# Optimization experiments

Measured on AMD Instinct MI355X. Metric: run time of the kernel, lower is better.

The kernel has to match this reference:

```python
import jax, jax.numpy as jnp
import numpy as np
from jax import lax

DN = ('NHWC', 'HWIO', 'NHWC')


def _conv(x, w, b=None, stride=1):
    y = lax.conv_general_dilated(x, w, (stride, stride), 'SAME', dimension_numbers=DN)
    return y + b if b is not None else y


def _conv_t(x, w, b, stride=2):
    y = lax.conv_transpose(x, w, (stride, stride), 'SAME', dimension_numbers=DN)
    return y + b


def _res_stack(x, blocks):
    # ResidualBlock: x + Conv1x1(relu(Conv3x3(relu(x)))); final relu after stack
    for w1, w2 in blocks:
        t = jax.nn.relu(x)
        t = _conv(t, w1)          # 3x3, no bias
        t = jax.nn.relu(t)
        t = _conv(t, w2)          # 1x1, no bias
        x = x + t
    return jax.nn.relu(x)


def setup_inputs() -> dict:
    key = jax.random.key(0)
    ks = jax.random.split(key, 32)
    s = 0.05
    n = lambda i, shape: jax.random.normal(ks[i], shape, dtype=jnp.float32) * s
    H, RH, D, K = 128, 32, 128, 512
    return {
        'x': jax.random.normal(ks[0], (16, 256, 256, 3), dtype=jnp.float32),
        'emb': jax.random.normal(ks[1], (K, D), dtype=jnp.float32),  # stddev 1.0 init
        'enc_w1': n(2, (4, 4, 3, H // 2)),  'enc_b1': jnp.zeros((H // 2,), jnp.float32),
        'enc_w2': n(3, (4, 4, H // 2, H)),  'enc_b2': jnp.zeros((H,), jnp.float32),
        'enc_w3': n(4, (3, 3, H, H)),       'enc_b3': jnp.zeros((H,), jnp.float32),
        'erb1_w1': n(5, (3, 3, H, RH)), 'erb1_w2': n(6, (1, 1, RH, H)),
        'erb2_w1': n(7, (3, 3, H, RH)), 'erb2_w2': n(8, (1, 1, RH, H)),
        'dec_w': n(9, (3, 3, D, H)),        'dec_b': jnp.zeros((H,), jnp.float32),
        'drb1_w1': n(10, (3, 3, H, RH)), 'drb1_w2': n(11, (1, 1, RH, H)),
        'drb2_w1': n(12, (3, 3, H, RH)), 'drb2_w2': n(13, (1, 1, RH, H)),
        'dt1_w': n(14, (4, 4, H, H // 2)),  'dt1_b': jnp.zeros((H // 2,), jnp.float32),
        'dt2_w': n(15, (4, 4, H // 2, 3)),  'dt2_b': jnp.zeros((3,), jnp.float32),
    }


def _forward(x, emb, enc_w1, enc_b1, enc_w2, enc_b2, enc_w3, enc_b3,
             erb1_w1, erb1_w2, erb2_w1, erb2_w2,
             dec_w, dec_b, drb1_w1, drb1_w2, drb2_w1, drb2_w2,
             dt1_w, dt1_b, dt2_w, dt2_b):
    f = jax.nn.relu(_conv(x, enc_w1, enc_b1, 2))
    f = jax.nn.relu(_conv(f, enc_w2, enc_b2, 2))
    f = _conv(f, enc_w3, enc_b3, 1)
    f = _res_stack(f, [(erb1_w1, erb1_w2), (erb2_w1, erb2_w2)])
    # VQ: full [N, K] squared-distance matrix, argmin, codebook gather
    D = emb.shape[1]
    flat = f.reshape(-1, D)                                   # [N, D]
    dist = ((flat ** 2).sum(axis=1, keepdims=True)
            + (emb ** 2).sum(axis=1)[None, :]
            - 2.0 * flat @ emb.T)                              # [N, K]
    idx = jnp.argmin(dist, axis=1)                             # [N]
    q = emb[idx].reshape(f.shape)                              # quantized
    y = _conv(q, dec_w, dec_b, 1)
    y = _res_stack(y, [(drb1_w1, drb1_w2), (drb2_w1, drb2_w2)])
    y = jax.nn.relu(_conv_t(y, dt1_w, dt1_b))
    y = _conv_t(y, dt2_w, dt2_b)
    return (y, f, q)


def reference(x, emb, enc_w1, enc_b1, enc_w2, enc_b2, enc_w3, enc_b3,
              erb1_w1, erb1_w2, erb2_w1, erb2_w2,
              dec_w, dec_b, drb1_w1, drb1_w2, drb2_w1, drb2_w2,
              dt1_w, dt1_b, dt2_w, dt2_b):
    return _forward(x, emb, enc_w1, enc_b1, enc_w2, enc_b2, enc_w3, enc_b3,
                    erb1_w1, erb1_w2, erb2_w1, erb2_w2,
                    dec_w, dec_b, drb1_w1, drb1_w2, drb2_w1, drb2_w2,
                    dt1_w, dt1_b, dt2_w, dt2_b)
```

## Files before the change

kernel.cpp:

```cpp
#include <hip/hip_runtime.h>
#include <hip/hip_bf16.h>
#include <hip/hip_fp16.h>

using bf16 = __hip_bfloat16;
using frag_ab = __attribute__((ext_vector_type(8))) short;
using f16x8  = __attribute__((ext_vector_type(8))) _Float16;
using frag_cd = __attribute__((ext_vector_type(4))) float;

enum { F_INRELU = 1, F_OUTRELU = 2, F_RES = 4 };

struct TapSet { int dy[16]; int dx[16]; int wi[16]; };

__device__ __forceinline__ unsigned int relu_pk(unsigned int v) {
    unsigned int m = ((v & 0x80008000u) >> 15) * 0xFFFFu;
    return v & ~m;
}
__device__ __forceinline__ unsigned int mask_by(unsigned int v, unsigned int h) {
    unsigned int m = ((h & 0x80008000u) >> 15) * 0xFFFFu;
    return v & ~m;
}

__global__ void pack_w_k(const float* __restrict__ w, bf16* __restrict__ dst,
                         int Ci, int Co, int BN, TapSet taps, int total)
{
    int idx = blockIdx.x * 256 + threadIdx.x;
    if (idx >= total) return;
    int j  = idx & 7;
    int r1 = idx >> 3;
    int nl = r1 % BN;
    int r2 = r1 / BN;
    int q  = r2 & 3;
    int cb = r2 >> 2;
    int nblocks = Co / BN;
    int c  = cb / nblocks;
    int nb = cb - c * nblocks;
    int cpt = Ci >> 5;
    int tap = c / cpt;
    int ci  = (c - tap * cpt) * 32 + q * 8 + j;
    int n   = nb * BN + nl;
    dst[idx] = __float2bfloat16(w[(size_t)(taps.wi[tap] * Ci + ci) * Co + n]);
}

__global__ void pack_w2_k(const float* __restrict__ w, __half* __restrict__ dst,
                          int Ci, int Co, int BN, TapSet taps, int total)
{
    int idx = blockIdx.x * 256 + threadIdx.x;
    if (idx >= total) return;
    int j  = idx & 7;
    int r1 = idx >> 3;
    int nl = r1 % BN;
    int r2 = r1 / BN;
    int q  = r2 & 3;
    int cb = r2 >> 2;
    int nblocks = Co / BN;
    int c  = cb / nblocks;
    int nb = cb - c * nblocks;
    int cpt = Ci >> 5;
    int tap = c / cpt;
    int ci  = (c - tap * cpt) * 32 + q * 8 + j;
    int n   = nb * BN + nl;
    float v = w[(size_t)(taps.wi[tap] * Ci + ci) * Co + n];
    __half h = __float2half(v);
    __half l = __float2half((v - __half2float(h)) * 2048.0f);
    size_t base = (size_t)cb * (BN * 64) + (q * BN + nl) * 8 + j;
    dst[base] = h;
    dst[base + BN * 32] = l;
}

__global__ void pack_wdt2_k(const float* __restrict__ w, __half* __restrict__ dst)
{
    int idx = blockIdx.x * 256 + threadIdx.x;
    if (idx >= 16384) return;
    int parity = idx >> 12;
    int r0 = idx & 4095;
    int j  = r0 & 7;
    int r1 = r0 >> 3;
    int nl = r1 & 15;
    int r2 = r1 >> 4;
    int q  = r2 & 3;
    int cb = r2 >> 2;
    int tap = cb >> 1;
    int cc  = cb & 1;
    int ci  = cc * 32 + q * 8 + j;
    int n   = nl;
    int py = parity >> 1, px = parity & 1;
    int ty = tap >> 1, tx = tap & 1;
    int wi = (py + 2 * ty) * 4 + (px + 2 * tx);
    float v = (n < 3) ? w[(size_t)(wi * 64 + ci) * 3 + n] : 0.f;
    __half h = __float2half(v);
    __half l = __float2half((v - __half2float(h)) * 2048.0f);
    size_t base = (size_t)parity * 8192 + cb * 1024 + (q * 16 + nl) * 8 + j;
    dst[base] = h;
    dst[base + 512] = l;
}

__global__ void pack_we1_k(const float* __restrict__ w, __half* __restrict__ dst)
{
    int idx = blockIdx.x * 256 + threadIdx.x;
    if (idx >= 4096) return;
    int j  = idx & 7;
    int r1 = idx >> 3;
    int nl = r1 & 63;
    int r2 = r1 >> 6;
    int q  = r2 & 3;
    int c  = r2 >> 2;
    int k  = c * 32 + q * 8 + j;
    int tap = k >> 2, ci = k & 3;
    float v = (ci < 3) ? w[(size_t)(tap * 3 + ci) * 64 + nl] : 0.f;
    __half h = __float2half(v);
    __half l = __float2half((v - __half2float(h)) * 2048.0f);
    size_t base = (size_t)c * 4096 + (q * 64 + nl) * 8 + j;
    dst[base] = h;
    dst[base + 2048] = l;
}

__global__ __launch_bounds__(256) void pad_x_k(
    const float* __restrict__ x, __half* __restrict__ xh, __half* __restrict__ xl)
{
    int pix = blockIdx.x * 256 + threadIdx.x;
    const float* ip = x + (size_t)pix * 3;
    float v0 = ip[0], v1 = ip[1], v2 = ip[2];
    unsigned short hb[4], lb[4];
    float vv[4] = {v0, v1, v2, 0.f};
#pragma unroll
    for (int i = 0; i < 4; ++i) {
        __half h = __float2half(vv[i]);
        hb[i] = __half_as_ushort(h);
        lb[i] = __half_as_ushort(__float2half((vv[i] - __half2float(h)) * 2048.0f));
    }
    uint2 hv = make_uint2((unsigned)hb[0] | ((unsigned)hb[1] << 16),
                          (unsigned)hb[2] | ((unsigned)hb[3] << 16));
    uint2 lv = make_uint2((unsigned)lb[0] | ((unsigned)lb[1] << 16),
                          (unsigned)lb[2] | ((unsigned)lb[3] << 16));
    *(uint2*)(xh + (size_t)pix * 4) = hv;
    *(uint2*)(xl + (size_t)pix * 4) = lv;
}

__global__ __launch_bounds__(256) void enc1_mfma_k(
    const __half* __restrict__ xh, const __half* __restrict__ xl,
    const __half* __restrict__ wp, const float* __restrict__ bias,
    __half* __restrict__ oh, __half* __restrict__ ol)
{
    __shared__ __align__(16) short Ash[64 * 32];
    __shared__ __align__(16) short Asl[64 * 32];
    __shared__ __align__(16) short Bsh[64 * 32];
    __shared__ __align__(16) short Bsl[64 * 32];

    const int tid = threadIdx.x;
    const int m0 = blockIdx.x * 64;

    const int am = tid >> 2;
    const int aq = tid & 3;
    const int gm  = m0 + am;
    const int nn_ = gm >> 14;
    const int rr_ = gm & 16383;
    const int iy0 = (rr_ >> 7) * 2 - 1;
    const int ix0 = (rr_ & 127) * 2 - 1;

    const int lane = tid & 63;
    const int wv4 = tid >> 6;
    const int wm = (wv4 & 1) * 32;
    const int wn = (wv4 >> 1) * 32;
    const int lm = lane & 15, lq = lane >> 4;

    frag_cd accA[2][2], accB[2][2];
#pragma unroll
    for (int i = 0; i < 2; ++i)
#pragma unroll
        for (int j = 0; j < 2; ++j)
#pragma unroll
            for (int r = 0; r < 4; ++r) { accA[i][j][r] = 0.f; accB[i][j][r] = 0.f; }

#pragma unroll
    for (int c = 0; c < 2; ++c) {
        const int tap = c * 8 + aq * 2;
        const int ky = tap >> 2, kx = tap & 3;
        const int iy = iy0 + ky;
        const int ix = ix0 + kx;
        uint2 h0 = make_uint2(0u, 0u), h1 = h0, l0 = h0, l1 = h0;
        if (iy >= 0 && iy < 256) {
            const size_t rowb = (size_t)(nn_ * 256 + iy) * 256;
            if (ix >= 0 && ix < 256) {
                h0 = *(const uint2*)(xh + (rowb + ix) * 4);
                l0 = *(const uint2*)(xl + (rowb + ix) * 4);
            }
            if (ix + 1 >= 0 && ix + 1 < 256) {
                h1 = *(const uint2*)(xh + (rowb + ix + 1) * 4);
                l1 = *(const uint2*)(xl + (rowb + ix + 1) * 4);
            }
        }
        __syncthreads();
        *(uint4*)&Ash[(aq * 64 + am) * 8] = make_uint4(h0.x, h0.y, h1.x, h1.y);
        *(uint4*)&Asl[(aq * 64 + am) * 8] = make_uint4(l0.x, l0.y, l1.x, l1.y);
        {
            const __half* wc = wp + (size_t)c * 4096;
            *(uint4*)&Bsh[tid * 8] = *(const uint4*)(wc + tid * 8);
            *(uint4*)&Bsl[tid * 8] = *(const uint4*)(wc + 2048 + tid * 8);
        }
        __syncthreads();

        f16x8 afh[2], afl[2], bfh[2], bfl[2];
#pragma unroll
        for (int i = 0; i < 2; ++i) {
            afh[i] = *(const f16x8*)&Ash[(lq * 64 + wm + i * 16 + lm) * 8];
            afl[i] = *(const f16x8*)&Asl[(lq * 64 + wm + i * 16 + lm) * 8];
        }
#pragma unroll
        for (int j = 0; j < 2; ++j) {
            bfh[j] = *(const f16x8*)&Bsh[(lq * 64 + wn + j * 16 + lm) * 8];
            bfl[j] = *(const f16x8*)&Bsl[(lq * 64 + wn + j * 16 + lm) * 8];
        }
#pragma unroll
        for (int i = 0; i < 2; ++i)
#pragma unroll
            for (int j = 0; j < 2; ++j) {
                accA[i][j] = __builtin_amdgcn_mfma_f32_16x16x32_f16(afh[i], bfh[j], accA[i][j], 0, 0, 0);
                accB[i][j] = __builtin_amdgcn_mfma_f32_16x16x32_f16(afh[i], bfl[j], accB[i][j], 0, 0, 0);
                accB[i][j] = __builtin_amdgcn_mfma_f32_16x16x32_f16(afl[i], bfh[j], accB[i][j], 0, 0, 0);
            }
    }

    const float s = 1.0f / 2048.0f;
#pragma unroll
    for (int j = 0; j < 2; ++j) {
        const int n_g = wn + j * 16 + lm;
        const float bv = bias[n_g];
#pragma unroll
        for (int i = 0; i < 2; ++i) {
#pragma unroll
            for (int r = 0; r < 4; ++r) {
                const int m_g = m0 + wm + i * 16 + lq * 4 + r;
                const size_t ob = (size_t)m_g * 64 + n_g;
                float v = accA[i][j][r] + accB[i][j][r] * s + bv;
                v = fmaxf(v, 0.f);
                __half h = __float2half(v);
                oh[ob] = h;
                ol[ob] = __float2half((v - __half2float(h)) * 2048.0f);
            }
        }
    }
}

template<int BN>
__global__ __launch_bounds__(256) void conv_mfma2_k(
    const __half* __restrict__ ah, const __half* __restrict__ al,
    const __half* __restrict__ wp, const float* __restrict__ bias,
    float* __restrict__ out, __half* __restrict__ oh, __half* __restrict__ ol,
    const __half* __restrict__ rh, const __half* __restrict__ rl,
    int IH, int IW, int Ci, int Co, int sy_in,
    TapSet taps, int ntaps, int flags)
{
    __shared__ __align__(16) short Ash[64 * 32];
    __shared__ __align__(16) short Asl[64 * 32];
    __shared__ __align__(16) short Bsh[BN * 32];
    __shared__ __align__(16) short Bsl[BN * 32];

    const int tid = threadIdx.x;
    const int m0 = blockIdx.x * 64;
    const int n0 = blockIdx.y * BN;

    const int am = tid >> 2;
    const int aq = tid & 3;
    const int gm  = m0 + am;
    const int nn_ = gm >> 12;
    const int rr_ = gm & 4095;
    const int oy_ = (rr_ >> 6) * sy_in;
    const int ox_ = (rr_ & 63) * sy_in;

    const int lane = tid & 63;
    const int wv4 = tid >> 6;
    constexpr int MT = (BN == 64) ? 2 : 1;
    constexpr int NT = 2;
    const int wm = (BN == 64) ? (wv4 & 1) * 32 : wv4 * 16;
    const int wn = (BN == 64) ? (wv4 >> 1) * 32 : 0;
    const int lm = lane & 15, lq = lane >> 4;
    constexpr int NLOAD = BN * 32 / 8;

    frag_cd accA[MT][NT], accB[MT][NT];
#pragma unroll
    for (int i = 0; i < MT; ++i)
#pragma unroll
        for (int j = 0; j < NT; ++j)
#pragma unroll
            for (int r = 0; r < 4; ++r) { accA[i][j][r] = 0.f; accB[i][j][r] = 0.f; }

    const int cpt = Ci >> 5;
    const int nch = ntaps * cpt;
    const bool inrelu = (flags & F_INRELU) != 0;

    int tap = 0, cc = 0, ci0 = 0;
    for (int c = 0; c < nch; ++c) {
        const int iy = oy_ + taps.dy[tap];
        const int ix = ox_ + taps.dx[tap];
        uint4 avh = make_uint4(0u, 0u, 0u, 0u);
        uint4 avl = make_uint4(0u, 0u, 0u, 0u);
        if (iy >= 0 && iy < IH && ix >= 0 && ix < IW) {
            const size_t off = (size_t)((nn_ * IH + iy) * IW + ix) * Ci + ci0 + aq * 8;
            avh = *(const uint4*)(ah + off);
            avl = *(const uint4*)(al + off);
        }
        if (inrelu) {
            avl.x = mask_by(avl.x, avh.x); avl.y = mask_by(avl.y, avh.y);
            avl.z = mask_by(avl.z, avh.z); avl.w = mask_by(avl.w, avh.w);
            avh.x = relu_pk(avh.x); avh.y = relu_pk(avh.y);
            avh.z = relu_pk(avh.z); avh.w = relu_pk(avh.w);
        }
        uint4 bvh, bvl;
        if (tid < NLOAD) {
            const __half* wc = wp + (size_t)(c * gridDim.y + blockIdx.y) * (BN * 64);
            bvh = *(const uint4*)(wc + tid * 8);
            bvl = *(const uint4*)(wc + BN * 32 + tid * 8);
        }

        __syncthreads();
        *(uint4*)&Ash[(aq * 64 + am) * 8] = avh;
        *(uint4*)&Asl[(aq * 64 + am) * 8] = avl;
        if (tid < NLOAD) {
            *(uint4*)&Bsh[tid * 8] = bvh;
            *(uint4*)&Bsl[tid * 8] = bvl;
        }
        __syncthreads();

        f16x8 afh[MT], afl[MT], bfh[NT], bfl[NT];
#pragma unroll
        for (int i = 0; i < MT; ++i) {
            afh[i] = *(const f16x8*)&Ash[(lq * 64 + wm + i * 16 + lm) * 8];
            afl[i] = *(const f16x8*)&Asl[(lq * 64 + wm + i * 16 + lm) * 8];
        }
#pragma unroll
        for (int j = 0; j < NT; ++j) {
            bfh[j] = *(const f16x8*)&Bsh[(lq * BN + wn + j * 16 + lm) * 8];
            bfl[j] = *(const f16x8*)&Bsl[(lq * BN + wn + j * 16 + lm) * 8];
        }
#pragma unroll
        for (int i = 0; i < MT; ++i)
#pragma unroll
            for (int j = 0; j < NT; ++j) {
                accA[i][j] = __builtin_amdgcn_mfma_f32_16x16x32_f16(afh[i], bfh[j], accA[i][j], 0, 0, 0);
                accB[i][j] = __builtin_amdgcn_mfma_f32_16x16x32_f16(afh[i], bfl[j], accB[i][j], 0, 0, 0);
                accB[i][j] = __builtin_amdgcn_mfma_f32_16x16x32_f16(afl[i], bfh[j], accB[i][j], 0, 0, 0);
            }

        ci0 += 32;
        if (++cc == cpt) { cc = 0; ci0 = 0; ++tap; }
    }

    const float s = 1.0f / 2048.0f;
#pragma unroll
    for (int j = 0; j < NT; ++j) {
        const int n_g = n0 + wn + j * 16 + lm;
        const float bv = bias ? bias[n_g] : 0.f;
#pragma unroll
        for (int i = 0; i < MT; ++i) {
#pragma unroll
            for (int r = 0; r < 4; ++r) {
                const int m_g = m0 + wm + i * 16 + lq * 4 + r;
                const size_t ob = (size_t)m_g * Co + n_g;
                float v = accA[i][j][r] + accB[i][j][r] * s + bv;
                if (flags & F_RES)
                    v += __half2float(rh[ob]) + __half2float(rl[ob]) * s;
                if (flags & F_OUTRELU) v = fmaxf(v, 0.f);
                if (out) out[ob] = v;
                if (oh) {
                    __half h = __float2half(v);
                    oh[ob] = h;
                    ol[ob] = __float2half((v - __half2float(h)) * 2048.0f);
                }
            }
        }
    }
}

template<int BN>
__global__ __launch_bounds__(256) void conv_mfma_k(
    const bf16* __restrict__ a, const bf16* __restrict__ wp,
    const float* __restrict__ bias,
    float* __restrict__ out, bf16* __restrict__ out_bf,
    const float* __restrict__ res,
    int Ci, int Co, int OHf, int OWf, int sy_out, int py, int px,
    TapSet taps, int ntaps, int flags)
{
    __shared__ __align__(16) short As[64 * 32];
    __shared__ __align__(16) short Bs[BN * 32];

    const int tid = threadIdx.x;
    const int m0 = blockIdx.x * 64;
    const int n0 = blockIdx.y * BN;

    const int am = tid >> 2;
    const int aq = tid & 3;
    const int gm  = m0 + am;
    const int nn_ = gm >> 12;
    const int rr_ = gm & 4095;
    const int oy_ = rr_ >> 6;
    const int ox_ = rr_ & 63;

    const int lane = tid & 63;
    const int wv4 = tid >> 6;
    constexpr int MT = (BN == 64) ? 2 : 1;
    constexpr int NT = 2;
    const int wm = (BN == 64) ? (wv4 & 1) * 32 : wv4 * 16;
    const int wn = (BN == 64) ? (wv4 >> 1) * 32 : 0;
    const int lm = lane & 15, lq = lane >> 4;
    constexpr int NLOAD = BN * 32 / 8;

    frag_cd acc[MT][NT];
#pragma unroll
    for (int i = 0; i < MT; ++i)
#pragma unroll
        for (int j = 0; j < NT; ++j)
#pragma unroll
            for (int r = 0; r < 4; ++r) acc[i][j][r] = 0.f;

    const int cpt = Ci >> 5;
    const int nch = ntaps * cpt;
    const bool inrelu = (flags & F_INRELU) != 0;

    int tap = 0, cc = 0, ci0 = 0;
    for (int c = 0; c < nch; ++c) {
        const int iy = oy_ + taps.dy[tap];
        const int ix = ox_ + taps.dx[tap];
        uint4 av = make_uint4(0u, 0u, 0u, 0u);
        if (iy >= 0 && iy < 64 && ix >= 0 && ix < 64)
            av = *(const uint4*)(a + (size_t)((nn_ * 64 + iy) * 64 + ix) * Ci + ci0 + aq * 8);
        if (inrelu) {
            av.x = relu_pk(av.x); av.y = relu_pk(av.y);
            av.z = relu_pk(av.z); av.w = relu_pk(av.w);
        }
        uint4 bv;
        if (tid < NLOAD)
            bv = *(const uint4*)(wp + ((size_t)c * gridDim.y + blockIdx.y) * (BN * 32) + tid * 8);

        __syncthreads();
        *(uint4*)&As[(aq * 64 + am) * 8] = av;
        if (tid < NLOAD) *(uint4*)&Bs[tid * 8] = bv;
        __syncthreads();

        frag_ab af[MT], bfr[NT];
#pragma unroll
        for (int i = 0; i < MT; ++i)
            af[i] = *(const frag_ab*)&As[(lq * 64 + wm + i * 16 + lm) * 8];
#pragma unroll
        for (int j = 0; j < NT; ++j)
            bfr[j] = *(const frag_ab*)&Bs[(lq * BN + wn + j * 16 + lm) * 8];
#pragma unroll
        for (int i = 0; i < MT; ++i)
#pragma unroll
            for (int j = 0; j < NT; ++j)
                acc[i][j] = __builtin_amdgcn_mfma_f32_16x16x32_bf16(af[i], bfr[j], acc[i][j], 0, 0, 0);

        ci0 += 32;
        if (++cc == cpt) { cc = 0; ci0 = 0; ++tap; }
    }

#pragma unroll
    for (int j = 0; j < NT; ++j) {
        const int n_g = n0 + wn + j * 16 + lm;
        const float bv = bias ? bias[n_g] : 0.f;
#pragma unroll
        for (int i = 0; i < MT; ++i) {
#pragma unroll
            for (int r = 0; r < 4; ++r) {
                const int m_g = m0 + wm + i * 16 + lq * 4 + r;
                const int nn2 = m_g >> 12;
                const int rr2 = m_g & 4095;
                const int oy = (rr2 >> 6) * sy_out + py;
                const int ox = (rr2 & 63) * sy_out + px;
                const size_t ob = ((size_t)(nn2 * OHf + oy) * OWf + ox) * Co + n_g;
                float v = acc[i][j][r] + bv;
                if (flags & F_RES)     v += res[ob];
                if (flags & F_OUTRELU) v = fmaxf(v, 0.f);
                if (out)    out[ob]    = v;
                if (out_bf) out_bf[ob] = __float2bfloat16(v);
            }
        }
    }
}

__global__ __launch_bounds__(256) void dt2_mfma_k(
    const float* __restrict__ in,
    const __half* __restrict__ wp,
    const float* __restrict__ bias,
    float* __restrict__ out)
{
    __shared__ __align__(16) short Ash[64 * 32];
    __shared__ __align__(16) short Asl[64 * 32];
    __shared__ __align__(16) short Bsh[16 * 32];
    __shared__ __align__(16) short Bsl[16 * 32];

    const int tid = threadIdx.x;
    const int par = blockIdx.x & 3;
    const int m0  = (blockIdx.x >> 2) * 64;
    const int py = par >> 1, px = par & 1;

    const int am = tid >> 2;
    const int aq = tid & 3;
    const int gm  = m0 + am;
    const int nn_ = gm >> 14;
    const int rr_ = gm & 16383;
    const int r_  = rr_ >> 7;
    const int c_  = rr_ & 127;

    const int lane = tid & 63;
    const int wv4 = tid >> 6;
    const int wm = wv4 * 16;
    const int lm = lane & 15, lq = lane >> 4;

    frag_cd accA, accB;
#pragma unroll
    for (int r = 0; r < 4; ++r) { accA[r] = 0.f; accB[r] = 0.f; }

    const __half* wpar = wp + (size_t)par * 8192;

    for (int c = 0; c < 8; ++c) {
        const int tap = c >> 1;
        const int iy = r_ + py + (tap >> 1) - 1;
        const int ix = c_ + px + (tap & 1) - 1;
        const int ci0 = (c & 1) * 32;
        uint4 hi = make_uint4(0u, 0u, 0u, 0u);
        uint4 lo = make_uint4(0u, 0u, 0u, 0u);
        if ((unsigned)iy < 128u && (unsigned)ix < 128u) {
            const float* ip = in + (size_t)((nn_ * 128 + iy) * 128 + ix) * 64 + ci0 + aq * 8;
            const float4 v0 = *(const float4*)ip;
            const float4 v1 = *(const float4*)(ip + 4);
            float vv[8] = {v0.x, v0.y, v0.z, v0.w, v1.x, v1.y, v1.z, v1.w};
            unsigned short hb[8], lb[8];
#pragma unroll
            for (int i = 0; i < 8; ++i) {
                __half h = __float2half(vv[i]);
                hb[i] = __half_as_ushort(h);
                lb[i] = __half_as_ushort(__float2half((vv[i] - __half2float(h)) * 2048.0f));
            }
            hi = make_uint4((unsigned)hb[0] | ((unsigned)hb[1] << 16),
                            (unsigned)hb[2] | ((unsigned)hb[3] << 16),
                            (unsigned)hb[4] | ((unsigned)hb[5] << 16),
                            (unsigned)hb[6] | ((unsigned)hb[7] << 16));
            lo = make_uint4((unsigned)lb[0] | ((unsigned)lb[1] << 16),
                            (unsigned)lb[2] | ((unsigned)lb[3] << 16),
                            (unsigned)lb[4] | ((unsigned)lb[5] << 16),
                            (unsigned)lb[6] | ((unsigned)lb[7] << 16));
        }
        uint4 bvh, bvl;
        if (tid < 64) {
            const __half* wc = wpar + c * 1024;
            bvh = *(const uint4*)(wc + tid * 8);
            bvl = *(const uint4*)(wc + 512 + tid * 8);
        }

        __syncthreads();
        *(uint4*)&Ash[(aq * 64 + am) * 8] = hi;
        *(uint4*)&Asl[(aq * 64 + am) * 8] = lo;
        if (tid < 64) {
            *(uint4*)&Bsh[tid * 8] = bvh;
            *(uint4*)&Bsl[tid * 8] = bvl;
        }
        __syncthreads();

        const f16x8 afh = *(const f16x8*)&Ash[(lq * 64 + wm + lm) * 8];
        const f16x8 afl = *(const f16x8*)&Asl[(lq * 64 + wm + lm) * 8];
        const f16x8 bfh = *(const f16x8*)&Bsh[(lq * 16 + lm) * 8];
        const f16x8 bfl = *(const f16x8*)&Bsl[(lq * 16 + lm) * 8];
        accA = __builtin_amdgcn_mfma_f32_16x16x32_f16(afh, bfh, accA, 0, 0, 0);
        accB = __builtin_amdgcn_mfma_f32_16x16x32_f16(afh, bfl, accB, 0, 0, 0);
        accB = __builtin_amdgcn_mfma_f32_16x16x32_f16(afl, bfh, accB, 0, 0, 0);
    }

    const float s = 1.0f / 2048.0f;
    if (lm < 3) {
        const float bv = bias[lm];
#pragma unroll
        for (int r = 0; r < 4; ++r) {
            const int m_g = m0 + wm + lq * 4 + r;
            const int nn2 = m_g >> 14;
            const int rr2 = m_g & 16383;
            const int oy = (rr2 >> 7) * 2 + py;
            const int ox = (rr2 & 127) * 2 + px;
            out[((size_t)(nn2 * 256 + oy) * 256 + ox) * 3 + lm] = accA[r] + accB[r] * s + bv;
        }
    }
}

__global__ void enorm_k(const float* __restrict__ emb, float* __restrict__ en) {
    int k = blockIdx.x * 256 + threadIdx.x;
    if (k >= 512) return;
    const float4* e = (const float4*)(emb + k * 128);
    float s = 0.f;
    for (int i = 0; i < 32; ++i) {
        float4 v = e[i];
        s += v.x * v.x + v.y * v.y + v.z * v.z + v.w * v.w;
    }
    en[k] = s;
}

__global__ void pack_emb_k(const float* __restrict__ emb, __half* __restrict__ dst)
{
    int idx = blockIdx.x * 256 + threadIdx.x;
    int k = idx & 127;
    int n = idx >> 7;
    float v = emb[idx];
    __half h = __float2half(v);
    __half l = __float2half((v - __half2float(h)) * 2048.0f);
    int nb = n >> 6, nl = n & 63;
    int ch = k >> 5, q = (k >> 3) & 3, j = k & 7;
    size_t base = (size_t)(nb * 4 + ch) * 4096 + (q * 64 + nl) * 8 + j;
    dst[base] = h;
    dst[base + 2048] = l;
}

__global__ __launch_bounds__(256) void vq_mfma_k(
    const __half* __restrict__ fh, const __half* __restrict__ fl,
    const __half* __restrict__ pe, const float* __restrict__ en,
    const float* __restrict__ emb, float* __restrict__ q, bf16* __restrict__ qb)
{
    __shared__ __align__(16) short Ash[64 * 128];
    __shared__ __align__(16) short Asl[64 * 128];
    __shared__ int sel[64];

    const int tid  = threadIdx.x;
    const int pos0 = blockIdx.x * 64;

    {
        const int am = tid >> 2;
        const int aq = tid & 3;
#pragma unroll
        for (int ch = 0; ch < 4; ++ch) {
            const size_t off = (size_t)(pos0 + am) * 128 + ch * 32 + aq * 8;
            uint4 vh = *(const uint4*)(fh + off);
            uint4 vl = *(const uint4*)(fl + off);
            *(uint4*)&Ash[((ch * 4 + aq) * 64 + am) * 8] = vh;
            *(uint4*)&Asl[((ch * 4 + aq) * 64 + am) * 8] = vl;
        }
    }
    __syncthreads();

    const int lane = tid & 63;
    const int w    = tid >> 6;
    const int lm = lane & 15, lq = lane >> 4;
    const int mbase = w * 16;
    const float s = 1.0f / 2048.0f;

    float best[4] = {3.4e38f, 3.4e38f, 3.4e38f, 3.4e38f};
    int   bidx[4] = {0, 0, 0, 0};

    f16x8 ah[4], alv[4];
#pragma unroll
    for (int ch = 0; ch < 4; ++ch) {
        ah[ch]  = *(const f16x8*)&Ash[((ch * 4 + lq) * 64 + mbase + lm) * 8];
        alv[ch] = *(const f16x8*)&Asl[((ch * 4 + lq) * 64 + mbase + lm) * 8];
    }

    for (int nb = 0; nb < 8; ++nb) {
        frag_cd accA[4], accB[4];
#pragma unroll
        for (int j = 0; j < 4; ++j)
#pragma unroll
            for (int r = 0; r < 4; ++r) { accA[j][r] = 0.f; accB[j][r] = 0.f; }

#pragma unroll
        for (int ch = 0; ch < 4; ++ch) {
            const __half* base = pe + (size_t)(nb * 4 + ch) * 4096;
            f16x8 bh[4], bl[4];
#pragma unroll
            for (int j = 0; j < 4; ++j) {
                const int o = (lq * 64 + j * 16 + lm) * 8;
                bh[j] = *(const f16x8*)(base + o);
                bl[j] = *(const f16x8*)(base + 2048 + o);
            }
#pragma unroll
            for (int j = 0; j < 4; ++j) {
                accA[j] = __builtin_amdgcn_mfma_f32_16x16x32_f16(ah[ch], bh[j], accA[j], 0, 0, 0);
                accB[j] = __builtin_amdgcn_mfma_f32_16x16x32_f16(ah[ch], bl[j], accB[j], 0, 0, 0);
                accB[j] = __builtin_amdgcn_mfma_f32_16x16x32_f16(alv[ch], bh[j], accB[j], 0, 0, 0);
            }
        }

#pragma unroll
        for (int j = 0; j < 4; ++j) {
            const int code = nb * 64 + j * 16 + lm;
            const float ec = en[code];
#pragma unroll
            for (int r = 0; r < 4; ++r) {
                float dot = accA[j][r] + accB[j][r] * s;
                float d = fmaf(dot, -2.f, ec);
                if (d < best[r]) { best[r] = d; bidx[r] = code; }
            }
        }
    }

#pragma unroll
    for (int r = 0; r < 4; ++r) {
        float d = best[r]; int ix = bidx[r];
#pragma unroll
        for (int m = 1; m < 16; m <<= 1) {
            float d2 = __shfl_xor(d, m);
            int   x2 = __shfl_xor(ix, m);
            if (d2 < d || (d2 == d && x2 < ix)) { d = d2; ix = x2; }
        }
        if (lm == 0) sel[mbase + lq * 4 + r] = ix;
    }
    __syncthreads();

#pragma unroll
    for (int jj = 0; jj < 32; ++jj) {
        int id = jj * 256 + tid;
        int p = id >> 7, k = id & 127;
        float v = emb[(size_t)sel[p] * 128 + k];
        q[(size_t)(pos0 + p) * 128 + k]  = v;
        qb[(size_t)(pos0 + p) * 128 + k] = __float2bfloat16(v);
    }
}

static TapSet conv_taps(int KH, int KW, int pad) {
    TapSet t{};
    for (int ky = 0; ky < KH; ++ky)
        for (int kx = 0; kx < KW; ++kx) {
            int i = ky * KW + kx;
            t.dy[i] = ky - pad; t.dx[i] = kx - pad; t.wi[i] = i;
        }
    return t;
}

static TapSet convt_taps(int py, int px) {
    TapSet t{};
    for (int ty = 0; ty < 2; ++ty)
        for (int tx = 0; tx < 2; ++tx) {
            int i = ty * 2 + tx;
            t.dy[i] = py + ty - 1;
            t.dx[i] = px + tx - 1;
            t.wi[i] = (py + 2 * ty) * 4 + (px + 2 * tx);
        }
    return t;
}

extern "C" void kernel_launch(void* const* d_in, const int* in_sizes, int n_in,
                              void* d_out, int out_size, void* d_ws, size_t ws_size,
                              hipStream_t stream)
{
    const float* x       = (const float*)d_in[0];
    const float* emb     = (const float*)d_in[1];
    const float* enc_w1  = (const float*)d_in[2];
    const float* enc_b1  = (const float*)d_in[3];
    const float* enc_w2  = (const float*)d_in[4];
    const float* enc_b2  = (const float*)d_in[5];
    const float* enc_w3  = (const float*)d_in[6];
    const float* enc_b3  = (const float*)d_in[7];
    const float* erb1_w1 = (const float*)d_in[8];
    const float* erb1_w2 = (const float*)d_in[9];
    const float* erb2_w1 = (const float*)d_in[10];
    const float* erb2_w2 = (const float*)d_in[11];
    const float* dec_w   = (const float*)d_in[12];
    const float* dec_b   = (const float*)d_in[13];
    const float* drb1_w1 = (const float*)d_in[14];
    const float* drb1_w2 = (const float*)d_in[15];
    const float* drb2_w1 = (const float*)d_in[16];
    const float* drb2_w2 = (const float*)d_in[17];
    const float* dt1_w   = (const float*)d_in[18];
    const float* dt1_b   = (const float*)d_in[19];
    const float* dt2_w   = (const float*)d_in[20];
    const float* dt2_b   = (const float*)d_in[21];

    char* wsb = (char*)d_ws;
    __half* H1 = (__half*)wsb;
    __half* L1 = (__half*)(wsb + (size_t)33554432);
    __half* H2 = (__half*)(wsb + (size_t)67108864);
    __half* L2 = (__half*)(wsb + (size_t)83886080);
    __half* Xh = (__half*)(wsb + (size_t)67108864);
    __half* Xl = (__half*)(wsb + (size_t)75497472);
    __half* H3 = (__half*)wsb;
    __half* L3 = (__half*)(wsb + (size_t)16777216);
    __half* H4 = (__half*)(wsb + (size_t)33554432);
    __half* L4 = (__half*)(wsb + (size_t)50331648);
    __half* Ht = (__half*)(wsb + (size_t)100663296);
    __half* Lt = (__half*)(wsb + (size_t)104857600);
    float*  EN = (float*)(wsb + (size_t)109051904);
    __half* Fh = (__half*)wsb;
    __half* Fl = (__half*)(wsb + (size_t)16777216);
    bf16* Qb  = (bf16*)(wsb + (size_t)67108864);
    bf16* Db  = (bf16*)(wsb + (size_t)83886080);
    bf16* Y1b = Qb;
    bf16* Y2b = Db;
    bf16* Tb  = (bf16*)(wsb + (size_t)100663296);
    float* Y0 = (float*)wsb;
    float* Y1 = (float*)(wsb + (size_t)33554432);
    float* A1 = (float*)wsb;
    char* pk = wsb + (size_t)109056000;
    bf16* Pdec  = (bf16*)pk;  pk += 147456 * 2;
    bf16* Pd1w1 = (bf16*)pk;  pk += 36864 * 2;
    bf16* Pd1w2 = (bf16*)pk;  pk += 4096 * 2;
    bf16* Pd2w1 = (bf16*)pk;  pk += 36864 * 2;
    bf16* Pd2w2 = (bf16*)pk;  pk += 4096 * 2;
    bf16* Pdt1[4];
    for (int i = 0; i < 4; ++i) { Pdt1[i] = (bf16*)pk; pk += 65536 * 2; }
    __half* P2enc2 = (__half*)pk; pk += 131072 * 4;
    __half* P2enc3 = (__half*)pk; pk += 147456 * 4;
    __half* P2e1w1 = (__half*)pk; pk += 36864 * 4;
    __half* P2e1w2 = (__half*)pk; pk += 4096 * 4;
    __half* P2e2w1 = (__half*)pk; pk += 36864 * 4;
    __half* P2e2w2 = (__half*)pk; pk += 4096 * 4;
    __half* Pe     = (__half*)pk; pk += 131072 * 2;
    __half* Pe1    = (__half*)pk; pk += 8192 * 2;
    __half* Pdt2   = (__half*)pk; pk += 32768 * 2;

    float* outY = (float*)d_out;
    float* outF = outY + 3145728;
    float* outQ = outF + 8388608;

    const TapSet t3 = conv_taps(3, 3, 1);
    const TapSet t4 = conv_taps(4, 4, 1);
    const TapSet t1 = conv_taps(1, 1, 0);
    TapSet tdt[4];
    for (int p = 0; p < 4; ++p) tdt[p] = convt_taps(p >> 1, p & 1);

    enorm_k<<<2, 256, 0, stream>>>(emb, EN);
    pack_emb_k<<<256, 256, 0, stream>>>(emb, Pe);
    pack_we1_k<<<16, 256, 0, stream>>>(enc_w1, Pe1);
    pack_wdt2_k<<<64, 256, 0, stream>>>(dt2_w, Pdt2);

    pack_w_k<<<(147456 + 255) / 256, 256, 0, stream>>>(dec_w, Pdec, 128, 128, 64, t3, 147456);
    pack_w_k<<<(36864 + 255) / 256, 256, 0, stream>>>(drb1_w1, Pd1w1, 128, 32, 32, t3, 36864);
    pack_w_k<<<(4096 + 255) / 256, 256, 0, stream>>>(drb1_w2, Pd1w2, 32, 128, 64, t1, 4096);
    pack_w_k<<<(36864 + 255) / 256, 256, 0, stream>>>(drb2_w1, Pd2w1, 128, 32, 32, t3, 36864);
    pack_w_k<<<(4096 + 255) / 256, 256, 0, stream>>>(drb2_w2, Pd2w2, 32, 128, 64, t1, 4096);
    for (int p = 0; p < 4; ++p)
        pack_w_k<<<(65536 + 255) / 256, 256, 0, stream>>>(dt1_w, Pdt1[p], 128, 64, 64, tdt[p], 65536);
    pack_w2_k<<<(131072 + 255) / 256, 256, 0, stream>>>(enc_w2, P2enc2, 64, 128, 64, t4, 131072);
    pack_w2_k<<<(147456 + 255) / 256, 256, 0, stream>>>(enc_w3, P2enc3, 128, 128, 64, t3, 147456);
    pack_w2_k<<<(36864 + 255) / 256, 256, 0, stream>>>(erb1_w1, P2e1w1, 128, 32, 32, t3, 36864);
    pack_w2_k<<<(4096 + 255) / 256, 256, 0, stream>>>(erb1_w2, P2e1w2, 32, 128, 64, t1, 4096);
    pack_w2_k<<<(36864 + 255) / 256, 256, 0, stream>>>(erb2_w1, P2e2w1, 128, 32, 32, t3, 36864);
    pack_w2_k<<<(4096 + 255) / 256, 256, 0, stream>>>(erb2_w2, P2e2w2, 32, 128, 64, t1, 4096);

    pad_x_k<<<4096, 256, 0, stream>>>(x, Xh, Xl);
    enc1_mfma_k<<<4096, 256, 0, stream>>>(Xh, Xl, Pe1, enc_b1, H1, L1);
    conv_mfma2_k<64><<<dim3(1024, 2), 256, 0, stream>>>(H1, L1, P2enc2, enc_b2,
        nullptr, H2, L2, nullptr, nullptr, 128, 128, 64, 128, 2, t4, 16, F_OUTRELU);
    conv_mfma2_k<64><<<dim3(1024, 2), 256, 0, stream>>>(H2, L2, P2enc3, enc_b3,
        nullptr, H3, L3, nullptr, nullptr, 64, 64, 128, 128, 1, t3, 9, 0);
    conv_mfma2_k<32><<<dim3(1024, 1), 256, 0, stream>>>(H3, L3, P2e1w1, nullptr,
        nullptr, Ht, Lt, nullptr, nullptr, 64, 64, 128, 32, 1, t3, 9, F_INRELU);
    conv_mfma2_k<64><<<dim3(1024, 2), 256, 0, stream>>>(Ht, Lt, P2e1w2, nullptr,
        nullptr, H4, L4, H3, L3, 64, 64, 32, 128, 1, t1, 1, F_INRELU | F_RES);
    conv_mfma2_k<32><<<dim3(1024, 1), 256, 0, stream>>>(H4, L4, P2e2w1, nullptr,
        nullptr, Ht, Lt, nullptr, nullptr, 64, 64, 128, 32, 1, t3, 9, F_INRELU);
    conv_mfma2_k<64><<<dim3(1024, 2), 256, 0, stream>>>(Ht, Lt, P2e2w2, nullptr,
        outF, Fh, Fl, H4, L4, 64, 64, 32, 128, 1, t1, 1, F_INRELU | F_RES | F_OUTRELU);

    vq_mfma_k<<<1024, 256, 0, stream>>>(Fh, Fl, Pe, EN, emb, outQ, Qb);

    conv_mfma_k<64><<<dim3(1024, 2), 256, 0, stream>>>(Qb, Pdec, dec_b, Y0, Db, nullptr,
        128, 128, 64, 64, 1, 0, 0, t3, 9, 0);
    conv_mfma_k<32><<<dim3(1024, 1), 256, 0, stream>>>(Db, Pd1w1, nullptr, nullptr, Tb, nullptr,
        128, 32, 64, 64, 1, 0, 0, t3, 9, F_INRELU);
    conv_mfma_k<64><<<dim3(1024, 2), 256, 0, stream>>>(Tb, Pd1w2, nullptr, Y1, Y1b, Y0,
        32, 128, 64, 64, 1, 0, 0, t1, 1, F_INRELU | F_RES);
    conv_mfma_k<32><<<dim3(1024, 1), 256, 0, stream>>>(Y1b, Pd2w1, nullptr, nullptr, Tb, nullptr,
        128, 32, 64, 64, 1, 0, 0, t3, 9, F_INRELU);
    conv_mfma_k<64><<<dim3(1024, 2), 256, 0, stream>>>(Tb, Pd2w2, nullptr, nullptr, Y2b, Y1,
        32, 128, 64, 64, 1, 0, 0, t1, 1, F_INRELU | F_RES | F_OUTRELU);
    for (int p = 0; p < 4; ++p)
        conv_mfma_k<64><<<dim3(1024, 1), 256, 0, stream>>>(Y2b, Pdt1[p], dt1_b, A1, nullptr, nullptr,
            128, 64, 128, 128, 2, p >> 1, p & 1, tdt[p], 4, F_OUTRELU);

    dt2_mfma_k<<<16384, 256, 0, stream>>>(A1, Pdt2, dt2_b, outY);
}
```

Baseline: 889.4 us.

## Use full-width 128-channel N tiles and XCD-aware block swizzle in conv kernels

Adds a BN=128 variant of the MFMA conv kernels, where each wave computes a 32x64 output tile, and switches all 128-output-channel convolutions to a single N-block grid. Each input activation tile is then loaded and ReLU-masked once instead of twice, at the cost of more accumulator registers per thread and possibly lower occupancy. It also remaps blockIdx.x with an XCD swizzle so that consecutive M tiles land on the same chiplet, with the aim of improving L2 locality of overlapping input halos.

```diff
diff --git a/kernel.cpp b/kernel.cpp
--- a/kernel.cpp
+++ b/kernel.cpp
@@ -18,6 +18,9 @@
 __device__ __forceinline__ unsigned int mask_by(unsigned int v, unsigned int h) {
     unsigned int m = ((h & 0x80008000u) >> 15) * 0xFFFFu;
     return v & ~m;
+}
+__device__ __forceinline__ int xcd_swz(int bx, int n) {
+    return (bx & 7) * (n >> 3) + (bx >> 3);
 }
 
 __global__ void pack_w_k(const float* __restrict__ w, bf16* __restrict__ dst,
@@ -147,7 +150,7 @@
     __shared__ __align__(16) short Bsl[64 * 32];
 
     const int tid = threadIdx.x;
-    const int m0 = blockIdx.x * 64;
+    const int m0 = xcd_swz(blockIdx.x, 4096) * 64;
 
     const int am = tid >> 2;
     const int aq = tid & 3;
@@ -256,7 +259,7 @@
     __shared__ __align__(16) short Bsl[BN * 32];
 
     const int tid = threadIdx.x;
-    const int m0 = blockIdx.x * 64;
+    const int m0 = xcd_swz(blockIdx.x, gridDim.x) * 64;
     const int n0 = blockIdx.y * BN;
 
     const int am = tid >> 2;
@@ -269,10 +272,10 @@
 
     const int lane = tid & 63;
     const int wv4 = tid >> 6;
-    constexpr int MT = (BN == 64) ? 2 : 1;
-    constexpr int NT = 2;
-    const int wm = (BN == 64) ? (wv4 & 1) * 32 : wv4 * 16;
-    const int wn = (BN == 64) ? (wv4 >> 1) * 32 : 0;
+    constexpr int MT = (BN >= 64) ? 2 : 1;
+    constexpr int NT = (BN == 128) ? 4 : 2;
+    const int wm = (BN >= 64) ? (wv4 & 1) * 32 : wv4 * 16;
+    const int wn = (BN == 128) ? (wv4 >> 1) * 64 : ((BN == 64) ? (wv4 >> 1) * 32 : 0);
     const int lm = lane & 15, lq = lane >> 4;
     constexpr int NLOAD = BN * 32 / 8;
 
@@ -305,19 +308,31 @@
             avh.x = relu_pk(avh.x); avh.y = relu_pk(avh.y);
             avh.z = relu_pk(avh.z); avh.w = relu_pk(avh.w);
         }
-        uint4 bvh, bvl;
-        if (tid < NLOAD) {
+        uint4 bvh0, bvl0, bvh1, bvl1;
+        {
             const __half* wc = wp + (size_t)(c * gridDim.y + blockIdx.y) * (BN * 64);
-            bvh = *(const uint4*)(wc + tid * 8);
-            bvl = *(const uint4*)(wc + BN * 32 + tid * 8);
+            if constexpr (BN == 128) {
+                bvh0 = *(const uint4*)(wc + tid * 8);
+                bvh1 = *(const uint4*)(wc + (256 + tid) * 8);
+                bvl0 = *(const uint4*)(wc + BN * 32 + tid * 8);
+                bvl1 = *(const uint4*)(wc + BN * 32 + (256 + tid) * 8);
+            } else if (tid < NLOAD) {
+                bvh0 = *(const uint4*)(wc + tid * 8);
+                bvl0 = *(const uint4*)(wc + BN * 32 + tid * 8);
+            }
         }
 
         __syncthreads();
         *(uint4*)&Ash[(aq * 64 + am) * 8] = avh;
         *(uint4*)&Asl[(aq * 64 + am) * 8] = avl;
-        if (tid < NLOAD) {
-            *(uint4*)&Bsh[tid * 8] = bvh;
-            *(uint4*)&Bsl[tid * 8] = bvl;
+        if constexpr (BN == 128) {
+            *(uint4*)&Bsh[tid * 8] = bvh0;
+            *(uint4*)&Bsh[(256 + tid) * 8] = bvh1;
+            *(uint4*)&Bsl[tid * 8] = bvl0;
+            *(uint4*)&Bsl[(256 + tid) * 8] = bvl1;
+        } else if (tid < NLOAD) {
+            *(uint4*)&Bsh[tid * 8] = bvh0;
+            *(uint4*)&Bsl[tid * 8] = bvl0;
         }
         __syncthreads();
 
@@ -384,7 +399,7 @@
     __shared__ __align__(16) short Bs[BN * 32];
 
     const int tid = threadIdx.x;
-    const int m0 = blockIdx.x * 64;
+    const int m0 = xcd_swz(blockIdx.x, gridDim.x) * 64;
     const int n0 = blockIdx.y * BN;
 
     const int am = tid >> 2;
@@ -397,10 +412,10 @@
 
     const int lane = tid & 63;
     const int wv4 = tid >> 6;
-    constexpr int MT = (BN == 64) ? 2 : 1;
-    constexpr int NT = 2;
-    const int wm = (BN == 64) ? (wv4 & 1) * 32 : wv4 * 16;
-    const int wn = (BN == 64) ? (wv4 >> 1) * 32 : 0;
+    constexpr int MT = (BN >= 64) ? 2 : 1;
+    constexpr int NT = (BN == 128) ? 4 : 2;
+    const int wm = (BN >= 64) ? (wv4 & 1) * 32 : wv4 * 16;
+    const int wn = (BN == 128) ? (wv4 >> 1) * 64 : ((BN == 64) ? (wv4 >> 1) * 32 : 0);
     const int lm = lane & 15, lq = lane >> 4;
     constexpr int NLOAD = BN * 32 / 8;
 
@@ -427,13 +442,25 @@
             av.x = relu_pk(av.x); av.y = relu_pk(av.y);
             av.z = relu_pk(av.z); av.w = relu_pk(av.w);
         }
-        uint4 bv;
-        if (tid < NLOAD)
-            bv = *(const uint4*)(wp + ((size_t)c * gridDim.y + blockIdx.y) * (BN * 32) + tid * 8);
+        uint4 bv0, bv1;
+        {
+            const bf16* wc = wp + ((size_t)c * gridDim.y + blockIdx.y) * (BN * 32);
+            if constexpr (BN == 128) {
+                bv0 = *(const uint4*)(wc + tid * 8);
+                bv1 = *(const uint4*)(wc + (256 + tid) * 8);
+            } else if (tid < NLOAD) {
+                bv0 = *(const uint4*)(wc + tid * 8);
+            }
+        }
 
         __syncthreads();
         *(uint4*)&As[(aq * 64 + am) * 8] = av;
-        if (tid < NLOAD) *(uint4*)&Bs[tid * 8] = bv;
+        if constexpr (BN == 128) {
+            *(uint4*)&Bs[tid * 8] = bv0;
+            *(uint4*)&Bs[(256 + tid) * 8] = bv1;
+        } else if (tid < NLOAD) {
+            *(uint4*)&Bs[tid * 8] = bv0;
+        }
         __syncthreads();
 
         frag_ab af[MT], bfr[NT];
@@ -489,8 +516,9 @@
     __shared__ __align__(16) short Bsl[16 * 32];
 
     const int tid = threadIdx.x;
-    const int par = blockIdx.x & 3;
-    const int m0  = (blockIdx.x >> 2) * 64;
+    const int bx  = xcd_swz(blockIdx.x, 16384);
+    const int par = bx & 3;
+    const int m0  = (bx >> 2) * 64;
     const int py = par >> 1, px = par & 1;
 
     const int am = tid >> 2;
@@ -816,46 +844,46 @@
     pack_we1_k<<<16, 256, 0, stream>>>(enc_w1, Pe1);
     pack_wdt2_k<<<64, 256, 0, stream>>>(dt2_w, Pdt2);
 
-    pack_w_k<<<(147456 + 255) / 256, 256, 0, stream>>>(dec_w, Pdec, 128, 128, 64, t3, 147456);
+    pack_w_k<<<(147456 + 255) / 256, 256, 0, stream>>>(dec_w, Pdec, 128, 128, 128, t3, 147456);
     pack_w_k<<<(36864 + 255) / 256, 256, 0, stream>>>(drb1_w1, Pd1w1, 128, 32, 32, t3, 36864);
-    pack_w_k<<<(4096 + 255) / 256, 256, 0, stream>>>(drb1_w2, Pd1w2, 32, 128, 64, t1, 4096);
+    pack_w_k<<<(4096 + 255) / 256, 256, 0, stream>>>(drb1_w2, Pd1w2, 32, 128, 128, t1, 4096);
     pack_w_k<<<(36864 + 255) / 256, 256, 0, stream>>>(drb2_w1, Pd2w1, 128, 32, 32, t3, 36864);
-    pack_w_k<<<(4096 + 255) / 256, 256, 0, stream>>>(drb2_w2, Pd2w2, 32, 128, 64, t1, 4096);
+    pack_w_k<<<(4096 + 255) / 256, 256, 0, stream>>>(drb2_w2, Pd2w2, 32, 128, 128, t1, 4096);
     for (int p = 0; p < 4; ++p)
         pack_w_k<<<(65536 + 255) / 256, 256, 0, stream>>>(dt1_w, Pdt1[p], 128, 64, 64, tdt[p], 65536);
-    pack_w2_k<<<(131072 + 255) / 256, 256, 0, stream>>>(enc_w2, P2enc2, 64, 128, 64, t4, 131072);
-    pack_w2_k<<<(147456 + 255) / 256, 256, 0, stream>>>(enc_w3, P2enc3, 128, 128, 64, t3, 147456);
+    pack_w2_k<<<(131072 + 255) / 256, 256, 0, stream>>>(enc_w2, P2enc2, 64, 128, 128, t4, 131072);
+    pack_w2_k<<<(147456 + 255) / 256, 256, 0, stream>>>(enc_w3, P2enc3, 128, 128, 128, t3, 147456);
     pack_w2_k<<<(36864 + 255) / 256, 256, 0, stream>>>(erb1_w1, P2e1w1, 128, 32, 32, t3, 36864);
-    pack_w2_k<<<(4096 + 255) / 256, 256, 0, stream>>>(erb1_w2, P2e1w2, 32, 128, 64, t1, 4096);
+    pack_w2_k<<<(4096 + 255) / 256, 256, 0, stream>>>(erb1_w2, P2e1w2, 32, 128, 128, t1, 4096);
     pack_w2_k<<<(36864 + 255) / 256, 256, 0, stream>>>(erb2_w1, P2e2w1, 128, 32, 32, t3, 36864);
-    pack_w2_k<<<(4096 + 255) / 256, 256, 0, stream>>>(erb2_w2, P2e2w2, 32, 128, 64, t1, 4096);
+    pack_w2_k<<<(4096 + 255) / 256, 256, 0, stream>>>(erb2_w2, P2e2w2, 32, 128, 128, t1, 4096);
 
     pad_x_k<<<4096, 256, 0, stream>>>(x, Xh, Xl);
     enc1_mfma_k<<<4096, 256, 0, stream>>>(Xh, Xl, Pe1, enc_b1, H1, L1);
-    conv_mfma2_k<64><<<dim3(1024, 2), 256, 0, stream>>>(H1, L1, P2enc2, enc_b2,
+    conv_mfma2_k<128><<<dim3(1024, 1), 256, 0, stream>>>(H1, L1, P2enc2, enc_b2,
         nullptr, H2, L2, nullptr, nullptr, 128, 128, 64, 128, 2, t4, 16, F_OUTRELU);
-    conv_mfma2_k<64><<<dim3(1024, 2), 256, 0, stream>>>(H2, L2, P2enc3, enc_b3,
+    conv_mfma2_k<128><<<dim3(1024, 1), 256, 0, stream>>>(H2, L2, P2enc3, enc_b3,
         nullptr, H3, L3, nullptr, nullptr, 64, 64, 128, 128, 1, t3, 9, 0);
     conv_mfma2_k<32><<<dim3(1024, 1), 256, 0, stream>>>(H3, L3, P2e1w1, nullptr,
         nullptr, Ht, Lt, nullptr, nullptr, 64, 64, 128, 32, 1, t3, 9, F_INRELU);
-    conv_mfma2_k<64><<<dim3(1024, 2), 256, 0, stream>>>(Ht, Lt, P2e1w2, nullptr,
+    conv_mfma2_k<128><<<dim3(1024, 1), 256, 0, stream>>>(Ht, Lt, P2e1w2, nullptr,
         nullptr, H4, L4, H3, L3, 64, 64, 32, 128, 1, t1, 1, F_INRELU | F_RES);
     conv_mfma2_k<32><<<dim3(1024, 1), 256, 0, stream>>>(H4, L4, P2e2w1, nullptr,
         nullptr, Ht, Lt, nullptr, nullptr, 64, 64, 128, 32, 1, t3, 9, F_INRELU);
-    conv_mfma2_k<64><<<dim3(1024, 2), 256, 0, stream>>>(Ht, Lt, P2e2w2, nullptr,
+    conv_mfma2_k<128><<<dim3(1024, 1), 256, 0, stream>>>(Ht, Lt, P2e2w2, nullptr,
         outF, Fh, Fl, H4, L4, 64, 64, 32, 128, 1, t1, 1, F_INRELU | F_RES | F_OUTRELU);
 
     vq_mfma_k<<<1024, 256, 0, stream>>>(Fh, Fl, Pe, EN, emb, outQ, Qb);
 
-    conv_mfma_k<64><<<dim3(1024, 2), 256, 0, stream>>>(Qb, Pdec, dec_b, Y0, Db, nullptr,
+    conv_mfma_k<128><<<dim3(1024, 1), 256, 0, stream>>>(Qb, Pdec, dec_b, Y0, Db, nullptr,
         128, 128, 64, 64, 1, 0, 0, t3, 9, 0);
     conv_mfma_k<32><<<dim3(1024, 1), 256, 0, stream>>>(Db, Pd1w1, nullptr, nullptr, Tb, nullptr,
         128, 32, 64, 64, 1, 0, 0, t3, 9, F_INRELU);
-    conv_mfma_k<64><<<dim3(1024, 2), 256, 0, stream>>>(Tb, Pd1w2, nullptr, Y1, Y1b, Y0,
+    conv_mfma_k<128><<<dim3(1024, 1), 256, 0, stream>>>(Tb, Pd1w2, nullptr, Y1, Y1b, Y0,
         32, 128, 64, 64, 1, 0, 0, t1, 1, F_INRELU | F_RES);
     conv_mfma_k<32><<<dim3(1024, 1), 256, 0, stream>>>(Y1b, Pd2w1, nullptr, nullptr, Tb, nullptr,
         128, 32, 64, 64, 1, 0, 0, t3, 9, F_INRELU);
-    conv_mfma_k<64><<<dim3(1024, 2), 256, 0, stream>>>(Tb, Pd2w2, nullptr, nullptr, Y2b, Y1,
+    conv_mfma_k<128><<<dim3(1024, 1), 256, 0, stream>>>(Tb, Pd2w2, nullptr, nullptr, Y2b, Y1,
         32, 128, 64, 64, 1, 0, 0, t1, 1, F_INRELU | F_RES | F_OUTRELU);
     for (int p = 0; p < 4; ++p)
         conv_mfma_k<64><<<dim3(1024, 1), 256, 0, stream>>>(Y2b, Pdt1[p], dt1_b, A1, nullptr, nullptr,
```

Result: faster. 834.0 us (-6.2%).
